# Performance work log

Measured on AMD Instinct MI355X. Metric: run time of the kernel, lower is better.

## Reference

```python
import jax, jax.numpy as jnp
import numpy as np

NAT, NN = 10000, 32
RSN, THETAN, NEMB = 16, 8, 4
RC = 5.0
ZETA = 16.0
FEAT = RSN * NEMB + RSN * THETAN * NEMB  # 576
PI = 3.141592653589793


def setup_inputs() -> dict:
    key = jax.random.key(0)
    ks = jax.random.split(key, 12)
    positions = jax.random.normal(ks[0], (NAT, 3), dtype=jnp.float32) * 2.0
    species_encoder = jax.random.normal(ks[1], (NAT, NEMB), dtype=jnp.float32)
    theta_s = jax.random.uniform(ks[2], (THETAN,), dtype=jnp.float32) * PI
    kn_rad = jnp.ones((1,), dtype=jnp.float32)
    neighbor_idx = jax.random.randint(ks[3], (NAT, NN), 0, NAT, dtype=jnp.int32)
    W1 = jax.random.normal(ks[4], (FEAT, 64), dtype=jnp.float32) / np.sqrt(FEAT)
    b1 = jnp.zeros((64,), dtype=jnp.float32)
    W2 = jax.random.normal(ks[5], (64, 64), dtype=jnp.float32) / 8.0
    b2 = jnp.zeros((64,), dtype=jnp.float32)
    W3 = jax.random.normal(ks[6], (64, 1), dtype=jnp.float32) / 8.0
    b3 = jnp.zeros((1,), dtype=jnp.float32)
    return {"positions": positions, "species_encoder": species_encoder,
            "theta_s": theta_s, "kn_rad": kn_rad,
            "W1": W1, "b1": b1, "W2": W2, "b2": b2, "W3": W3, "b3": b3,
            "neighbor_idx": neighbor_idx}


def _bessel_radial(rnorm, kn_rad):
    # spherical-Bessel radial basis with smooth cosine cutoff (help_fn.bessel_function)
    fc = 0.5 * (jnp.cos(PI * rnorm / RC) + 1.0) * (rnorm < RC).astype(rnorm.dtype)
    k = jnp.arange(1, RSN + 1, dtype=rnorm.dtype)                     # [RSN]
    arg = (PI / RC) * kn_rad[0] * k[None, None, :] * rnorm[..., None]  # [nat,NN,RSN]
    return jnp.sqrt(2.0 / RC) * jnp.sin(arg) / rnorm[..., None] * fc[..., None]


def reference(positions, species_encoder, theta_s, kn_rad,
              W1, b1, W2, b2, W3, b3, neighbor_idx):
    # gather neighbor displacements: [nat, NN, 3]
    rij = positions[neighbor_idx] - positions[:, None, :]
    rnorm = jnp.linalg.norm(rij, axis=-1) + 1e-8                      # [nat, NN]

    bf = _bessel_radial(rnorm, kn_rad)                                # [nat, NN, RSN]
    # center-x-neighbor species embedding product (einsum 'ijk->ik->ijk')
    semb_ij = species_encoder[neighbor_idx] * species_encoder[:, None, :]  # [nat,NN,NEMB]

    # radial descriptors: [nat, RSN, NEMB] -> [nat, RSN*NEMB]
    desc_rad = jnp.einsum('ijl,ijm->ilm', bf, semb_ij).reshape(NAT, -1)

    # angular part
    rij_unit = rij / rnorm[..., None]
    cos_ijk = jnp.einsum('ijc,ikc->ijk', rij_unit, rij_unit)          # [nat,NN,NN]
    cos_ijk = jnp.clip(cos_ijk, -1.0 + 1e-6, 1.0 - 1e-6)
    sin_ijk = jnp.sqrt(1.0 - cos_ijk * cos_ijk)
    ct, st = jnp.cos(theta_s), jnp.sin(theta_s)

    # factorized per-bond channel tensor P: [nat, NN, RSN*NEMB]
    P = jnp.einsum('ijl,ijm->ijlm', bf, semb_ij).reshape(NAT, NN, RSN * NEMB)
    pref = 2.0 ** (1.0 - ZETA)
    ang = []
    for t in range(THETAN):  # small fixed loop over angle centers
        cosd = cos_ijk * ct[t] + sin_ijk * st[t]                      # cos(theta - theta_s)
        A = pref * (1.0 + cosd) ** ZETA                               # [nat,NN,NN]
        C = jnp.einsum('ijk,ijp->ikp', A, P)                          # contract over j
        ang.append(jnp.sum(C * P, axis=1))                            # [nat, RSN*NEMB]
    desc_ang = jnp.stack(ang, axis=1).reshape(NAT, -1)                # [nat, THETAN*RSN*NEMB]

    desc = jnp.concatenate([desc_rad, desc_ang], axis=1)              # [nat, FEAT]

    # per-atom MLP -> atomic energies, scatter-sum to total energy
    h = jnp.tanh(desc @ W1 + b1)
    h = jnp.tanh(h @ W2 + b2)
    e_atom = (h @ W3 + b3)[:, 0]                                      # [nat]
    return jnp.sum(e_atom)
```

## Files before the change

kernel.cpp:

```cpp
#include <hip/hip_runtime.h>
#include <hip/hip_bf16.h>

#define NATC 10000
#define NNC 32
#define RSNC 16
#define THETANC 8
#define NEMBC 4
#define FEATC 576

typedef __attribute__((ext_vector_type(8))) short short8;
typedef __attribute__((ext_vector_type(4))) float f32x4;

static __device__ __forceinline__ short f2bf(float x) {
    union { __hip_bfloat16 h; short s; } u;
    u.h = __float2bfloat16(x);
    return u.s;
}

__global__ __launch_bounds__(256) void prep_kernel(
    const float* __restrict__ W1, ushort* __restrict__ W1p)
{
    const int gid = blockIdx.x * 256 + threadIdx.x;
    const int l = gid & 63, ntks = gid >> 6;
    const int nt = ntks & 3, ks = ntks >> 2;
    const int q = l >> 4, c = l & 15;
    ushort pk[8];
    #pragma unroll
    for (int jj = 0; jj < 8; ++jj)
        pk[jj] = (ushort)f2bf(W1[(ks * 32 + q * 8 + jj) * 64 + nt * 16 + c]);
    #pragma unroll
    for (int jj = 0; jj < 8; ++jj) W1p[gid * 8 + jj] = pk[jj];
}

__global__ __launch_bounds__(256, 4) void desc_kernel(
    const float* __restrict__ pos,
    const float* __restrict__ spe,
    const float* __restrict__ theta_s,
    const float* __restrict__ kn_rad,
    const int* __restrict__ nidx,
    const ushort* __restrict__ W1p,
    const float* __restrict__ b1,
    const float* __restrict__ W2,
    const float* __restrict__ b2,
    const float* __restrict__ W3,
    const float* __restrict__ b3,
    float* __restrict__ e_atom)
{
    constexpr float RC = 5.0f;
    constexpr float PI_F = 3.14159265358979323846f;
    constexpr float PREF = 3.0517578125e-05f;

    __shared__ __attribute__((aligned(16))) float ux[NNC], uy[NNC], uz[NNC];
    __shared__ __attribute__((aligned(16))) float rbase[NNC], rw[NNC];
    __shared__ __attribute__((aligned(16))) float bfs[NNC * 17];
    __shared__ __attribute__((aligned(16))) float ses[NNC * 5];
    __shared__ __attribute__((aligned(16))) float P[NNC * 66];
    __shared__ __attribute__((aligned(16))) float cosm[NNC * 33];
    __shared__ __attribute__((aligned(16))) float sinm[NNC * 33];
    __shared__ __attribute__((aligned(16))) short Pb[4 * 64 * 8];
    __shared__ __attribute__((aligned(16))) ushort drow[FEATC];
    __shared__ __attribute__((aligned(16))) float h1p[64];
    __shared__ __attribute__((aligned(16))) float h1f[64];

    const int i   = blockIdx.x;
    const int tid = threadIdx.x;

    if (tid < NNC) {
        const int j = tid;
        const int n = nidx[i * NNC + j];
        const float pix = pos[i * 3 + 0], piy = pos[i * 3 + 1], piz = pos[i * 3 + 2];
        const float dx = pos[n * 3 + 0] - pix;
        const float dy = pos[n * 3 + 1] - piy;
        const float dz = pos[n * 3 + 2] - piz;
        const float r = sqrtf(dx * dx + dy * dy + dz * dz) + 1e-8f;
        const float inv = 1.0f / r;
        ux[j] = dx * inv; uy[j] = dy * inv; uz[j] = dz * inv;
        const float fc = (r < RC) ? 0.5f * (cosf(PI_F * r * (1.0f / RC)) + 1.0f) : 0.0f;
        rbase[j] = sqrtf(2.0f / RC) * inv * fc;
        rw[j]    = (PI_F / RC) * kn_rad[0] * r;
        #pragma unroll
        for (int m = 0; m < NEMBC; ++m)
            ses[j * 5 + m] = spe[n * NEMBC + m] * spe[i * NEMBC + m];
    }
    __syncthreads();

    #pragma unroll
    for (int k = 0; k < 2; ++k) {
        const int e = tid + k * 256;
        const int j = e >> 4, l = e & 15;
        bfs[j * 17 + l] = rbase[j] * sinf(rw[j] * (float)(l + 1));
    }
    __syncthreads();

    #pragma unroll
    for (int k = 0; k < 8; ++k) {
        const int e = tid + k * 256;
        const int j = e >> 6, p = e & 63;
        P[j * 66 + p] = bfs[j * 17 + (p >> 2)] * ses[j * 5 + (p & 3)];
    }
    #pragma unroll
    for (int k = 0; k < 4; ++k) {
        const int idx = tid + k * 256;
        const int j = idx >> 5, kk = idx & 31;
        float c = ux[j] * ux[kk] + uy[j] * uy[kk] + uz[j] * uz[kk];
        c = fminf(fmaxf(c, -1.0f + 1e-6f), 1.0f - 1e-6f);
        cosm[j * 33 + kk] = c;
        sinm[j * 33 + kk] = sqrtf(fmaxf(1.0f - c * c, 0.0f));
    }
    __syncthreads();

    {
        const int nt = tid >> 6, l2 = tid & 63;
        const int q2 = l2 >> 4, c2 = l2 & 15;
        short8 pk;
        #pragma unroll
        for (int jj = 0; jj < 8; ++jj)
            pk[jj] = f2bf(P[(q2 * 8 + jj) * 66 + nt * 16 + c2]);
        *(short8*)&Pb[(nt * 64 + l2) * 8] = pk;
    }
    if (tid < 64) {
        float s = 0.0f;
        #pragma unroll 8
        for (int j = 0; j < NNC; ++j) s += P[j * 66 + tid];
        drow[tid] = (ushort)f2bf(s);
    }
    __syncthreads();

    const int w = tid >> 6, l = tid & 63;
    const int q = l >> 4, c = l & 15;

    for (int tt = 0; tt < 2; ++tt) {
        const int t = w + tt * 4;
        const float th = theta_s[t];
        const float ct = cosf(th), st = sinf(th);

        short8 afr[2];
        #pragma unroll
        for (int mt = 0; mt < 2; ++mt) {
            const int kk = mt * 16 + c;
            #pragma unroll
            for (int jj = 0; jj < 8; ++jj) {
                const int j = q * 8 + jj;
                const float cv = cosm[kk * 33 + j];
                const float sv = sinm[kk * 33 + j];
                const float cosd = fmaf(cv, ct, sv * st);
                const float x = 1.0f + cosd;
                const float x2 = x * x, x4 = x2 * x2, x8 = x4 * x4;
                afr[mt][jj] = f2bf(PREF * (x8 * x8));
            }
        }

        f32x4 acc[2][4];
        #pragma unroll
        for (int mt = 0; mt < 2; ++mt)
            #pragma unroll
            for (int nt = 0; nt < 4; ++nt)
                acc[mt][nt] = (f32x4){0.0f, 0.0f, 0.0f, 0.0f};

        #pragma unroll
        for (int nt = 0; nt < 4; ++nt) {
            const short8 bfr = *(const short8*)&Pb[(nt * 64 + l) * 8];
            acc[0][nt] = __builtin_amdgcn_mfma_f32_16x16x32_bf16(afr[0], bfr, acc[0][nt], 0, 0, 0);
            acc[1][nt] = __builtin_amdgcn_mfma_f32_16x16x32_bf16(afr[1], bfr, acc[1][nt], 0, 0, 0);
        }

        float pt[4];
        #pragma unroll
        for (int nt = 0; nt < 4; ++nt) {
            float s = 0.0f;
            #pragma unroll
            for (int mt = 0; mt < 2; ++mt)
                #pragma unroll
                for (int r = 0; r < 4; ++r) {
                    const int kk = mt * 16 + q * 4 + r;
                    s = fmaf(acc[mt][nt][r], P[kk * 66 + nt * 16 + c], s);
                }
            s += __shfl_xor(s, 16, 64);
            s += __shfl_xor(s, 32, 64);
            pt[nt] = s;
        }
        const float v = (q == 0) ? pt[0] : (q == 1) ? pt[1] : (q == 2) ? pt[2] : pt[3];
        drow[64 + t * 64 + l] = (ushort)f2bf(v);
    }
    __syncthreads();

    {
        f32x4 acc1 = (f32x4){0.0f, 0.0f, 0.0f, 0.0f};
        const short8 zero8 = (short8){0, 0, 0, 0, 0, 0, 0, 0};
        #pragma unroll 3
        for (int ks = 0; ks < 18; ++ks) {
            const short8 bfr = *(const short8*)&W1p[((ks * 4 + w) * 64 + l) * 8];
            short8 afr = *(const short8*)&drow[ks * 32 + q * 8];
            if (c != 0) afr = zero8;
            acc1 = __builtin_amdgcn_mfma_f32_16x16x32_bf16(afr, bfr, acc1, 0, 0, 0);
        }
        if (l < 16) h1p[w * 16 + l] = acc1[0];
    }
    __syncthreads();

    if (tid < 64) {
        h1f[tid] = tanhf(h1p[tid] + b1[tid]);
        float acc2 = b2[tid];
        #pragma unroll 8
        for (int k = 0; k < 64; ++k)
            acc2 = fmaf(h1f[k], W2[k * 64 + tid], acc2);
        float s = tanhf(acc2) * W3[tid];
        #pragma unroll
        for (int off = 1; off <= 32; off <<= 1)
            s += __shfl_xor(s, off, 64);
        if (tid == 0) e_atom[i] = s + b3[0];
    }
}

__global__ __launch_bounds__(256) void reduce_kernel(
    const float* __restrict__ e_atom, float* __restrict__ out)
{
    __shared__ float red[4];
    const int tid = threadIdx.x;
    float s = 0.0f;
    for (int idx = tid; idx < NATC / 4; idx += 256) {
        const float4 v = *(const float4*)&e_atom[idx * 4];
        s += (v.x + v.y) + (v.z + v.w);
    }
    #pragma unroll
    for (int off = 1; off <= 32; off <<= 1)
        s += __shfl_xor(s, off, 64);
    if ((tid & 63) == 0) red[tid >> 6] = s;
    __syncthreads();
    if (tid == 0) out[0] = (red[0] + red[1]) + (red[2] + red[3]);
}

extern "C" void kernel_launch(void* const* d_in, const int* in_sizes, int n_in,
                              void* d_out, int out_size, void* d_ws, size_t ws_size,
                              hipStream_t stream)
{
    const float* pos   = (const float*)d_in[0];
    const float* spe   = (const float*)d_in[1];
    const float* theta = (const float*)d_in[2];
    const float* kn    = (const float*)d_in[3];
    const float* W1    = (const float*)d_in[4];
    const float* b1    = (const float*)d_in[5];
    const float* W2    = (const float*)d_in[6];
    const float* b2    = (const float*)d_in[7];
    const float* W3    = (const float*)d_in[8];
    const float* b3    = (const float*)d_in[9];
    const int*   nidx  = (const int*)d_in[10];
    float* out = (float*)d_out;

    float*  e_atom = (float*)d_ws;
    ushort* W1p    = (ushort*)((char*)d_ws + 40000);

    prep_kernel<<<18, 256, 0, stream>>>(W1, W1p);
    desc_kernel<<<NATC, 256, 0, stream>>>(pos, spe, theta, kn, nidx,
                                          W1p, b1, W2, b2, W3, b3, e_atom);
    reduce_kernel<<<1, 256, 0, stream>>>(e_atom, out);
}
```

Baseline: 155.0 us.

## Fuse final reduction via last-block atomic, MFMA second MLP layer, vectorize cos/sin loads

Removes the separate reduce kernel launch by having the last finishing block, detected through an atomic counter reset in the prep kernel, sum all atomic energies. The second MLP layer moves from a 64-thread scalar FMA loop over fp32 W2 to bf16 MFMA using a W2 matrix pre-packed in the prep kernel. The cos/sin matrices are padded to a stride of 36 so they can be read with float4 loads. This trades extra bf16 rounding in layer two and atomic/fence overhead for fewer launches and less per-block serial work.

```diff
diff --git a/kernel.cpp b/kernel.cpp
--- a/kernel.cpp
+++ b/kernel.cpp
@@ -18,18 +18,24 @@
 }
 
 __global__ __launch_bounds__(256) void prep_kernel(
-    const float* __restrict__ W1, ushort* __restrict__ W1p)
+    const float* __restrict__ W1, const float* __restrict__ W2,
+    ushort* __restrict__ W1p, ushort* __restrict__ W2p,
+    unsigned int* __restrict__ counter)
 {
     const int gid = blockIdx.x * 256 + threadIdx.x;
-    const int l = gid & 63, ntks = gid >> 6;
+    if (gid == 0) *counter = 0u;
+    const float* W = (gid < 4608) ? W1 : W2;
+    ushort* Wp = (gid < 4608) ? W1p : W2p;
+    const int g = (gid < 4608) ? gid : gid - 4608;
+    const int l = g & 63, ntks = g >> 6;
     const int nt = ntks & 3, ks = ntks >> 2;
     const int q = l >> 4, c = l & 15;
     ushort pk[8];
     #pragma unroll
     for (int jj = 0; jj < 8; ++jj)
-        pk[jj] = (ushort)f2bf(W1[(ks * 32 + q * 8 + jj) * 64 + nt * 16 + c]);
-    #pragma unroll
-    for (int jj = 0; jj < 8; ++jj) W1p[gid * 8 + jj] = pk[jj];
+        pk[jj] = (ushort)f2bf(W[(ks * 32 + q * 8 + jj) * 64 + nt * 16 + c]);
+    #pragma unroll
+    for (int jj = 0; jj < 8; ++jj) Wp[g * 8 + jj] = pk[jj];
 }
 
 __global__ __launch_bounds__(256, 4) void desc_kernel(
@@ -40,11 +46,13 @@
     const int* __restrict__ nidx,
     const ushort* __restrict__ W1p,
     const float* __restrict__ b1,
-    const float* __restrict__ W2,
+    const ushort* __restrict__ W2p,
     const float* __restrict__ b2,
     const float* __restrict__ W3,
     const float* __restrict__ b3,
-    float* __restrict__ e_atom)
+    float* __restrict__ e_atom,
+    unsigned int* __restrict__ counter,
+    float* __restrict__ out)
 {
     constexpr float RC = 5.0f;
     constexpr float PI_F = 3.14159265358979323846f;
@@ -55,12 +63,14 @@
     __shared__ __attribute__((aligned(16))) float bfs[NNC * 17];
     __shared__ __attribute__((aligned(16))) float ses[NNC * 5];
     __shared__ __attribute__((aligned(16))) float P[NNC * 66];
-    __shared__ __attribute__((aligned(16))) float cosm[NNC * 33];
-    __shared__ __attribute__((aligned(16))) float sinm[NNC * 33];
+    __shared__ __attribute__((aligned(16))) float cosm[NNC * 36];
+    __shared__ __attribute__((aligned(16))) float sinm[NNC * 36];
     __shared__ __attribute__((aligned(16))) short Pb[4 * 64 * 8];
     __shared__ __attribute__((aligned(16))) ushort drow[FEATC];
     __shared__ __attribute__((aligned(16))) float h1p[64];
-    __shared__ __attribute__((aligned(16))) float h1f[64];
+    __shared__ __attribute__((aligned(16))) ushort h1b[64];
+    __shared__ float red[4];
+    __shared__ int lastflag;
 
     const int i   = blockIdx.x;
     const int tid = threadIdx.x;
@@ -104,8 +114,8 @@
         const int j = idx >> 5, kk = idx & 31;
         float c = ux[j] * ux[kk] + uy[j] * uy[kk] + uz[j] * uz[kk];
         c = fminf(fmaxf(c, -1.0f + 1e-6f), 1.0f - 1e-6f);
-        cosm[j * 33 + kk] = c;
-        sinm[j * 33 + kk] = sqrtf(fmaxf(1.0f - c * c, 0.0f));
+        cosm[j * 36 + kk] = c;
+        sinm[j * 36 + kk] = sqrtf(fmaxf(1.0f - c * c, 0.0f));
     }
     __syncthreads();
 
@@ -138,12 +148,18 @@
         #pragma unroll
         for (int mt = 0; mt < 2; ++mt) {
             const int kk = mt * 16 + c;
+            const float4 c0 = *(const float4*)&cosm[kk * 36 + q * 8];
+            const float4 c1 = *(const float4*)&cosm[kk * 36 + q * 8 + 4];
+            const float4 s0 = *(const float4*)&sinm[kk * 36 + q * 8];
+            const float4 s1 = *(const float4*)&sinm[kk * 36 + q * 8 + 4];
+            float cv[8], sv[8];
+            cv[0]=c0.x; cv[1]=c0.y; cv[2]=c0.z; cv[3]=c0.w;
+            cv[4]=c1.x; cv[5]=c1.y; cv[6]=c1.z; cv[7]=c1.w;
+            sv[0]=s0.x; sv[1]=s0.y; sv[2]=s0.z; sv[3]=s0.w;
+            sv[4]=s1.x; sv[5]=s1.y; sv[6]=s1.z; sv[7]=s1.w;
             #pragma unroll
             for (int jj = 0; jj < 8; ++jj) {
-                const int j = q * 8 + jj;
-                const float cv = cosm[kk * 33 + j];
-                const float sv = sinm[kk * 33 + j];
-                const float cosd = fmaf(cv, ct, sv * st);
+                const float cosd = fmaf(cv[jj], ct, sv[jj] * st);
                 const float x = 1.0f + cosd;
                 const float x2 = x * x, x4 = x2 * x2, x8 = x4 * x4;
                 afr[mt][jj] = f2bf(PREF * (x8 * x8));
@@ -198,36 +214,49 @@
     }
     __syncthreads();
 
-    if (tid < 64) {
-        h1f[tid] = tanhf(h1p[tid] + b1[tid]);
-        float acc2 = b2[tid];
-        #pragma unroll 8
-        for (int k = 0; k < 64; ++k)
-            acc2 = fmaf(h1f[k], W2[k * 64 + tid], acc2);
-        float s = tanhf(acc2) * W3[tid];
+    if (tid < 64) h1b[tid] = (ushort)f2bf(tanhf(h1p[tid] + b1[tid]));
+    __syncthreads();
+    {
+        f32x4 acc2 = (f32x4){0.0f, 0.0f, 0.0f, 0.0f};
+        const short8 zero8 = (short8){0, 0, 0, 0, 0, 0, 0, 0};
+        #pragma unroll
+        for (int ks = 0; ks < 2; ++ks) {
+            const short8 bfr = *(const short8*)&W2p[((ks * 4 + w) * 64 + l) * 8];
+            short8 afr = *(const short8*)&h1b[ks * 32 + q * 8];
+            if (c != 0) afr = zero8;
+            acc2 = __builtin_amdgcn_mfma_f32_16x16x32_bf16(afr, bfr, acc2, 0, 0, 0);
+        }
+        float s = 0.0f;
+        if (l < 16) s = tanhf(acc2[0] + b2[w * 16 + l]) * W3[w * 16 + l];
+        s += __shfl_xor(s, 1, 64);
+        s += __shfl_xor(s, 2, 64);
+        s += __shfl_xor(s, 4, 64);
+        s += __shfl_xor(s, 8, 64);
+        if (l == 0) red[w] = s;
+    }
+    __syncthreads();
+
+    if (tid == 0) {
+        e_atom[i] = (red[0] + red[1]) + (red[2] + red[3]) + b3[0];
+        __threadfence();
+        const unsigned int old = atomicAdd(counter, 1u);
+        lastflag = (old == (unsigned int)(NATC - 1)) ? 1 : 0;
+    }
+    __syncthreads();
+    if (lastflag) {
+        __threadfence();
+        float s = 0.0f;
+        for (int idx = tid; idx < NATC / 4; idx += 256) {
+            const float4 v = *(const float4*)&e_atom[idx * 4];
+            s += (v.x + v.y) + (v.z + v.w);
+        }
         #pragma unroll
         for (int off = 1; off <= 32; off <<= 1)
             s += __shfl_xor(s, off, 64);
-        if (tid == 0) e_atom[i] = s + b3[0];
-    }
-}
-
-__global__ __launch_bounds__(256) void reduce_kernel(
-    const float* __restrict__ e_atom, float* __restrict__ out)
-{
-    __shared__ float red[4];
-    const int tid = threadIdx.x;
-    float s = 0.0f;
-    for (int idx = tid; idx < NATC / 4; idx += 256) {
-        const float4 v = *(const float4*)&e_atom[idx * 4];
-        s += (v.x + v.y) + (v.z + v.w);
-    }
-    #pragma unroll
-    for (int off = 1; off <= 32; off <<= 1)
-        s += __shfl_xor(s, off, 64);
-    if ((tid & 63) == 0) red[tid >> 6] = s;
-    __syncthreads();
-    if (tid == 0) out[0] = (red[0] + red[1]) + (red[2] + red[3]);
+        if ((tid & 63) == 0) red[tid >> 6] = s;
+        __syncthreads();
+        if (tid == 0) out[0] = (red[0] + red[1]) + (red[2] + red[3]);
+    }
 }
 
 extern "C" void kernel_launch(void* const* d_in, const int* in_sizes, int n_in,
@@ -247,11 +276,13 @@
     const int*   nidx  = (const int*)d_in[10];
     float* out = (float*)d_out;
 
-    float*  e_atom = (float*)d_ws;
-    ushort* W1p    = (ushort*)((char*)d_ws + 40000);
-
-    prep_kernel<<<18, 256, 0, stream>>>(W1, W1p);
+    float*        e_atom  = (float*)d_ws;
+    ushort*       W1p     = (ushort*)((char*)d_ws + 40064);
+    ushort*       W2p     = W1p + 4608 * 8;
+    unsigned int* counter = (unsigned int*)(W2p + 512 * 8);
+
+    prep_kernel<<<20, 256, 0, stream>>>(W1, W2, W1p, W2p, counter);
     desc_kernel<<<NATC, 256, 0, stream>>>(pos, spe, theta, kn, nidx,
-                                          W1p, b1, W2, b2, W3, b3, e_atom);
-    reduce_kernel<<<1, 256, 0, stream>>>(e_atom, out);
-}
+                                          W1p, b1, W2p, b2, W3, b3,
+                                          e_atom, counter, out);
+}
```

Result: slower. 286.6 us (+84.9%).
